# Optimization experiments

Hardware: AMD Instinct MI355X
Metric: run time of the kernel (lower is better)

## Reference

```python
import jax, jax.numpy as jnp
import numpy as np

B, T, F = 512, 1024, 8
H1, H2 = 70, 21   # '80k' config, bidirectional
D1, D2 = 30, 20


def _u(key, shape, fan):
    s = 1.0 / np.sqrt(fan)
    return jax.random.uniform(key, shape, jnp.float32, -s, s)


def setup_inputs() -> dict:
    key = jax.random.key(0)
    ks = iter(jax.random.split(key, 32))
    inp = {"x": jax.random.normal(next(ks), (B, T, F), jnp.float32)}
    # LSTM layer 1 (input F -> H1), forward and backward directions; torch gate order i,f,g,o
    for d in ("f", "b"):
        inp[f"w_ih1_{d}"] = _u(next(ks), (4 * H1, F), H1)
        inp[f"w_hh1_{d}"] = _u(next(ks), (4 * H1, H1), H1)
        inp[f"b_ih1_{d}"] = _u(next(ks), (4 * H1,), H1)
        inp[f"b_hh1_{d}"] = _u(next(ks), (4 * H1,), H1)
    # LSTM layer 2 (input 2*H1 -> H2)
    for d in ("f", "b"):
        inp[f"w_ih2_{d}"] = _u(next(ks), (4 * H2, 2 * H1), H2)
        inp[f"w_hh2_{d}"] = _u(next(ks), (4 * H2, H2), H2)
        inp[f"b_ih2_{d}"] = _u(next(ks), (4 * H2,), H2)
        inp[f"b_hh2_{d}"] = _u(next(ks), (4 * H2,), H2)
    # Dense head: 2*H2 -> D1 -> D2 -> 1
    inp["d1_w"] = _u(next(ks), (D1, 2 * H2), 2 * H2)
    inp["d1_b"] = _u(next(ks), (D1,), 2 * H2)
    inp["d2_w"] = _u(next(ks), (D2, D1), D1)
    inp["d2_b"] = _u(next(ks), (D2,), D1)
    inp["out_w"] = _u(next(ks), (1, D2), D2)
    inp["out_b"] = _u(next(ks), (1,), D2)
    return inp


def _lstm_dir(x, w_ih, w_hh, b_ih, b_hh, reverse):
    # x: [B, T, Fin]; torch LSTM gate order: i, f, g, o
    if reverse:
        x = x[:, ::-1]
    H = w_hh.shape[1]
    pre = jnp.einsum('btf,gf->btg', x, w_ih) + b_ih + b_hh  # [B, T, 4H]
    pre_t = jnp.moveaxis(pre, 1, 0)                          # [T, B, 4H]

    def step(carry, p):
        h, c = carry
        g = p + h @ w_hh.T
        i, f, gg, o = jnp.split(g, 4, axis=-1)
        c = jax.nn.sigmoid(f) * c + jax.nn.sigmoid(i) * jnp.tanh(gg)
        h = jax.nn.sigmoid(o) * jnp.tanh(c)
        return (h, c), h

    init = (jnp.zeros((x.shape[0], H), x.dtype), jnp.zeros((x.shape[0], H), x.dtype))
    _, hs = jax.lax.scan(step, init, pre_t)
    hs = jnp.moveaxis(hs, 0, 1)  # [B, T, H]
    if reverse:
        hs = hs[:, ::-1]
    return hs


def _bilstm(x, wf, uf, bif, bhf, wb, ub, bib, bhb):
    return jnp.concatenate([
        _lstm_dir(x, wf, uf, bif, bhf, reverse=False),
        _lstm_dir(x, wb, ub, bib, bhb, reverse=True),
    ], axis=-1)


def reference(x,
              w_ih1_f, w_hh1_f, b_ih1_f, b_hh1_f,
              w_ih1_b, w_hh1_b, b_ih1_b, b_hh1_b,
              w_ih2_f, w_hh2_f, b_ih2_f, b_hh2_f,
              w_ih2_b, w_hh2_b, b_ih2_b, b_hh2_b,
              d1_w, d1_b, d2_w, d2_b, out_w, out_b):
    h = _bilstm(x, w_ih1_f, w_hh1_f, b_ih1_f, b_hh1_f,
                w_ih1_b, w_hh1_b, b_ih1_b, b_hh1_b)   # [B, T, 2*H1]
    h = _bilstm(h, w_ih2_f, w_hh2_f, b_ih2_f, b_hh2_f,
                w_ih2_b, w_hh2_b, b_ih2_b, b_hh2_b)   # [B, T, 2*H2]
    h = jax.nn.relu(h @ d1_w.T + d1_b)
    h = jax.nn.relu(h @ d2_w.T + d2_b)
    return h @ out_w.T + out_b                          # [B, T, 1]
```

## Files before the change

kernel.cpp:

```cpp
#include <hip/hip_runtime.h>


typedef _Float16 v2f16 __attribute__((ext_vector_type(2)));
typedef _Float16 v4h   __attribute__((ext_vector_type(4)));
typedef _Float16 v8h   __attribute__((ext_vector_type(8)));
typedef float    f32x4 __attribute__((ext_vector_type(4)));

__device__ __forceinline__ float fdot2(v2f16 a, v2f16 b, float c) {
  return __builtin_amdgcn_fdot2(a, b, c, false);
}
#if __has_builtin(__builtin_amdgcn_rcpf)
__device__ __forceinline__ float rcpf(float x) { return __builtin_amdgcn_rcpf(x); }
#else
__device__ __forceinline__ float rcpf(float x) { return 1.f / x; }
#endif
__device__ __forceinline__ float ex2(float v) {
#if __has_builtin(__builtin_amdgcn_exp2f)
  return __builtin_amdgcn_exp2f(v);
#else
  return __expf(v * 0.6931471805599453f);
#endif
}

__device__ __forceinline__ void lds_barrier() {
  asm volatile("s_waitcnt lgkmcnt(0)" ::: "memory");
  __builtin_amdgcn_s_barrier();
  __builtin_amdgcn_sched_barrier(0);
}

#define O_W1M  0u
#define O_WP2  110592u
#define O_W2M  118656u
#define O_BIAS 177792u
#define O_DATA 178496u

__global__ void pack_kernel(const float* __restrict__ wihf, const float* __restrict__ whhf,
                            const float* __restrict__ wihb, const float* __restrict__ whhb,
                            const float* __restrict__ b1if, const float* __restrict__ b1hf,
                            const float* __restrict__ b1ib, const float* __restrict__ b1hb,
                            const float* __restrict__ wih2f, const float* __restrict__ wih2b,
                            const float* __restrict__ whh2f, const float* __restrict__ whh2b,
                            const float* __restrict__ bif, const float* __restrict__ bhf,
                            const float* __restrict__ bib, const float* __restrict__ bhb,
                            char* __restrict__ ws) {
  _Float16* w1m = (_Float16*)(ws + O_W1M);
  _Float16* wp2 = (_Float16*)(ws + O_WP2);
  _Float16* w2m = (_Float16*)(ws + O_W2M);
  float* biasc = (float*)(ws + O_BIAS);
  int idx = blockIdx.x * 256 + threadIdx.x;
  if (idx < 55296) {
    int d = idx / 27648, rem = idx % 27648, rp = rem / 96, k = rem % 96;
    int u = rp >> 2, g = rp & 3;
    const float* wih = d ? wihb : wihf;
    const float* whh = d ? whhb : whhf;
    const float* bi = d ? b1ib : b1if;
    const float* bh = d ? b1hb : b1hf;
    float v = 0.f;
    if (u < 70) {
      int src = g * 70 + u;
      float scale = (g == 2) ? 2.8853900817779268f : 1.4426950408889634f;
      if (k < 8) v = wih[src * 8 + k] * scale;
      else if (k < 78) v = whh[src * 70 + (k - 8)] * scale;
      else if (k == 78) v = (bi[src] + bh[src]) * scale;
    }
    w1m[idx] = (_Float16)v;
  } else if (idx < 59328) {
    int j = idx - 55296;
    int d = j / 2016, rem = j % 2016, r = rem / 24, k = rem % 24;
    const float* whh = d ? whh2b : whh2f;
    wp2[j] = (_Float16)((k < 21) ? whh[r * 21 + k] : 0.f);
  } else if (idx < 88896) {
    int j = idx - 59328;
    int n = j / 168, k = j % 168;
    float v = 0.f;
    if (k < 140) {
      if (n < 84) v = wih2f[n * 140 + k];
      else if (n < 168) v = wih2b[(n - 84) * 140 + k];
    }
    w2m[j] = (_Float16)v;
  } else if (idx < 89072) {
    int n = idx - 88896;
    float v = 0.f;
    if (n < 84) v = bif[n] + bhf[n];
    else if (n < 168) v = bib[n - 84] + bhb[n - 84];
    biasc[n] = v;
  }
}

__global__ __launch_bounds__(768) void lstm1_kernel(
    const float* __restrict__ x,
    const _Float16* __restrict__ w1m,
    _Float16* __restrict__ h1, int b0, int nb) {
  __shared__ __align__(16) _Float16 km[2][16][104];
  const int tid = threadIdx.x;
  const int w = tid >> 6, lane = tid & 63;
  const int q = lane >> 4, bc = lane & 15;
  const int d = blockIdx.y;
  const int blg = blockIdx.x * 16;
  const int gb0 = b0 + blg;

  for (int i = tid; i < 2 * 16 * 104; i += 768) ((_Float16*)km)[i] = (_Float16)0.f;

  int nt, T0;
  if (w < 4)       { nt = 1; T0 = w; }
  else if (w < 10) { nt = 2; T0 = 4 + 2 * (w - 4); }
  else             { nt = 1; T0 = 16 + (w - 10); }

  v8h af[2][3];
#pragma unroll
  for (int i = 0; i < 2; ++i) {
    if (i < nt) {
      int T = T0 + i;
#pragma unroll
      for (int kc = 0; kc < 3; ++kc)
        af[i][kc] = *(const v8h*)&w1m[(size_t)(d * 288 + T * 16 + bc) * 96 + kc * 32 + q * 8];
    }
  }

  __syncthreads();

  if (tid < 16) {
    km[0][tid][78] = (_Float16)1.f;
    km[1][tid][78] = (_Float16)1.f;
  }
  if (tid < 32) {
    int b = tid >> 1, half = tid & 1;
    int t0 = d ? 1023 : 0;
    float4 xv = *(const float4*)&x[((size_t)(gb0 + b) * 1024 + t0) * 8 + half * 4];
    v4h xh; xh[0] = (_Float16)xv.x; xh[1] = (_Float16)xv.y;
    xh[2] = (_Float16)xv.z; xh[3] = (_Float16)xv.w;
    *(v4h*)&km[0][b][half * 4] = xh;
  }
  float c0 = 0.f, c1 = 0.f;
  __syncthreads();

#pragma unroll 1
  for (int s = 0; s < 1024; ++s) {
    const int cur = s & 1, nxt = cur ^ 1;
    float4 xv;
    const bool xl = (tid < 32) && (s < 1023);
    if (xl) {
      int tn = d ? (1022 - s) : (s + 1);
      xv = *(const float4*)&x[((size_t)(gb0 + (tid >> 1)) * 1024 + tn) * 8 + (tid & 1) * 4];
    }
    v8h bf0 = *(const v8h*)&km[cur][bc][q * 8];
    v8h bf1 = *(const v8h*)&km[cur][bc][32 + q * 8];
    v8h bf2 = *(const v8h*)&km[cur][bc][64 + q * 8];
    f32x4 z4 = (f32x4){0.f, 0.f, 0.f, 0.f};
    f32x4 A0 = __builtin_amdgcn_mfma_f32_16x16x32_f16(af[0][0], bf0, z4, 0, 0, 0);
    f32x4 A1 = z4;
    if (nt == 2) A1 = __builtin_amdgcn_mfma_f32_16x16x32_f16(af[1][0], bf0, z4, 0, 0, 0);
    A0 = __builtin_amdgcn_mfma_f32_16x16x32_f16(af[0][1], bf1, A0, 0, 0, 0);
    if (nt == 2) A1 = __builtin_amdgcn_mfma_f32_16x16x32_f16(af[1][1], bf1, A1, 0, 0, 0);
    A0 = __builtin_amdgcn_mfma_f32_16x16x32_f16(af[0][2], bf2, A0, 0, 0, 0);
    if (nt == 2) A1 = __builtin_amdgcn_mfma_f32_16x16x32_f16(af[1][2], bf2, A1, 0, 0, 0);
    const int te = d ? (1023 - s) : s;
    const size_t rowb = ((size_t)te * nb + blg + bc) * 176 + d * 70;

#define GATE(Ai, ci, U)                                                      \
    {                                                                        \
      float ei = ex2(-Ai[0]);                                                \
      float ef = ex2(-Ai[1]);                                                \
      float eg = ex2(-Ai[2]);                                                \
      float eo = ex2(-Ai[3]);                                                \
      float si = rcpf(1.f + ei);                                             \
      float sf = rcpf(1.f + ef);                                             \
      float tg = fmaf(2.f, rcpf(1.f + eg), -1.f);                            \
      float so = rcpf(1.f + eo);                                             \
      ci = fmaf(sf, ci, si * tg);                                            \
      float ec = ex2(ci * -2.8853900817779268f);                             \
      float hv = so * fmaf(2.f, rcpf(1.f + ec), -1.f);                       \
      if ((U) < 70) {                                                        \
        _Float16 hh = (_Float16)hv;                                          \
        km[nxt][bc][8 + (U)] = hh;                                           \
        h1[rowb + (U)] = hh;                                                 \
      }                                                                      \
    }
    GATE(A0, c0, T0 * 4 + q)
    if (nt == 2) GATE(A1, c1, (T0 + 1) * 4 + q)
#undef GATE
    if (xl) {
      v4h xh; xh[0] = (_Float16)xv.x; xh[1] = (_Float16)xv.y;
      xh[2] = (_Float16)xv.z; xh[3] = (_Float16)xv.w;
      *(v4h*)&km[nxt][tid >> 1][(tid & 1) * 4] = xh;
    }
    lds_barrier();
  }
}

__global__ __launch_bounds__(256) void pre2_kernel(
    _Float16* __restrict__ h1, const char* __restrict__ ws) {
  const _Float16* w2m = (const _Float16*)(ws + O_W2M);
  const float* biasc = (const float*)(ws + O_BIAS);
  __shared__ _Float16 Al[64][184];
  __shared__ float Bl[176];
  const int tid = threadIdx.x;
  const int r0 = blockIdx.x * 64;
#pragma unroll
  for (int i = 0; i < 6; ++i) {
    int cid = i * 256 + tid;
    if (cid < 1408) {
      int row = cid / 22, ch = cid % 22;
      *(v8h*)&Al[row][ch * 8] = *(const v8h*)&h1[(size_t)(r0 + row) * 176 + ch * 8];
    }
  }
  if (tid < 176) Bl[tid] = biasc[tid];
  __syncthreads();

  const int wv = tid >> 6, lane = tid & 63;
  const int ml = lane & 15, kq = lane >> 4;
  v8h af[5];
#pragma unroll
  for (int k = 0; k < 4; ++k)
    af[k] = *(const v8h*)&Al[wv * 16 + ml][k * 32 + kq * 8];
  {
    v8h a4 = *(const v8h*)&Al[wv * 16 + ml][128 + kq * 8];
    if (kq >= 2) {
#pragma unroll
      for (int j = 0; j < 8; ++j) a4[j] = (_Float16)0.f;
    } else if (kq == 1) {
#pragma unroll
      for (int j = 4; j < 8; ++j) a4[j] = (_Float16)0.f;
    }
    af[4] = a4;
  }

  const v8h* wg = (const v8h*)w2m;
  f32x4 acc[11];
#pragma unroll
  for (int ct = 0; ct < 11; ++ct) acc[ct] = (f32x4){0.f, 0.f, 0.f, 0.f};

  v8h bc[5], bn[5];
#pragma unroll
  for (int k = 0; k < 5; ++k) bn[k] = wg[(size_t)ml * 21 + k * 4 + kq];
#pragma unroll
  for (int ct = 0; ct < 11; ++ct) {
#pragma unroll
    for (int k = 0; k < 5; ++k) bc[k] = bn[k];
    if (ct < 10) {
#pragma unroll
      for (int k = 0; k < 5; ++k) bn[k] = wg[(size_t)((ct + 1) * 16 + ml) * 21 + k * 4 + kq];
    }
#pragma unroll
    for (int k = 0; k < 5; ++k)
      acc[ct] = __builtin_amdgcn_mfma_f32_16x16x32_f16(af[k], bc[k], acc[ct], 0, 0, 0);
  }
  __syncthreads();
#pragma unroll
  for (int ct = 0; ct < 11; ++ct) {
#pragma unroll
    for (int r = 0; r < 4; ++r) {
      int row = wv * 16 + kq * 4 + r, col = ct * 16 + ml;
      Al[row][col] = (_Float16)(acc[ct][r] + Bl[col]);
    }
  }
  __syncthreads();
#pragma unroll
  for (int i = 0; i < 6; ++i) {
    int cid = i * 256 + tid;
    if (cid < 1408) {
      int row = cid / 22, ch = cid % 22;
      *(v8h*)&h1[(size_t)(r0 + row) * 176 + ch * 8] = *(const v8h*)&Al[row][ch * 8];
    }
  }
}

__global__ __launch_bounds__(64) void lstm2_kernel(
    const _Float16* __restrict__ pre2, const _Float16* __restrict__ wp2,
    _Float16* __restrict__ h2, int nb) {
  __shared__ __align__(16) _Float16 kv[2][32];
  const int lane = threadIdx.x;
  const int bl = blockIdx.x;
  const int d = blockIdx.y;
  const int u = lane >> 1, p = lane & 1;
  const bool active = lane < 42;

  ((_Float16*)kv)[lane] = (_Float16)0.f;

  v2f16 w0[12], w1[12];
  if (active) {
    const v8h* wr0 = (const v8h*)&wp2[(d * 84 + (2 * p) * 21 + u) * 24];
    const v8h* wr1 = (const v8h*)&wp2[(d * 84 + (2 * p + 1) * 21 + u) * 24];
#pragma unroll
    for (int ch = 0; ch < 3; ++ch) {
      v8h a = wr0[ch], b = wr1[ch];
#pragma unroll
      for (int q = 0; q < 4; ++q) {
        v2f16 t0; t0[0] = a[2 * q]; t0[1] = a[2 * q + 1]; w0[ch * 4 + q] = t0;
        v2f16 t1; t1[0] = b[2 * q]; t1[1] = b[2 * q + 1]; w1[ch * 4 + q] = t1;
      }
    }
  }
  const int col0 = d * 84 + (2 * p) * 21 + u;
  const int col1 = col0 + 21;
  const ptrdiff_t dlt = (ptrdiff_t)(d ? -nb : nb) * 176;
  const _Float16* pp = pre2 + ((size_t)(d ? 1023 : 0) * (size_t)nb + bl) * 176;

  _Float16 pa0 = pp[col0],            pa1 = pp[col1];
  _Float16 pb0 = (pp + dlt)[col0],    pb1 = (pp + dlt)[col1];
  _Float16 pc0 = (pp + 2*dlt)[col0],  pc1 = (pp + 2*dlt)[col1];
  _Float16 pd0 = (pp + 3*dlt)[col0],  pd1 = (pp + 3*dlt)[col1];
  const _Float16* pf = pp + 4 * dlt;

  const float esc0 = p ? -2.f : -1.f;
  const float ym0  = p ?  2.f :  1.f;
  const float ya0  = p ? -1.f :  0.f;
  float cc = 0.f;
  int s = 0;

#define L2STEP(P0, P1)                                                      \
  {                                                                         \
    const int cur = s & 1, nxt = cur ^ 1;                                   \
    float A0v = (float)P0, A1v = (float)P1;                                 \
    const float4* kp = (const float4*)&kv[cur][0];                          \
    float4 q0 = kp[0], q1 = kp[1], q2 = kp[2];                              \
    float x0 = A0v, x1 = 0.f, x2 = 0.f, x3 = 0.f;                           \
    float z0 = A1v, z1 = 0.f, z2 = 0.f, z3 = 0.f;                           \
    x0 = fdot2(__builtin_bit_cast(v2f16, q0.x), w0[0], x0);                 \
    x1 = fdot2(__builtin_bit_cast(v2f16, q0.y), w0[1], x1);                 \
    x2 = fdot2(__builtin_bit_cast(v2f16, q0.z), w0[2], x2);                 \
    x3 = fdot2(__builtin_bit_cast(v2f16, q0.w), w0[3], x3);                 \
    x0 = fdot2(__builtin_bit_cast(v2f16, q1.x), w0[4], x0);                 \
    x1 = fdot2(__builtin_bit_cast(v2f16, q1.y), w0[5], x1);                 \
    x2 = fdot2(__builtin_bit_cast(v2f16, q1.z), w0[6], x2);                 \
    x3 = fdot2(__builtin_bit_cast(v2f16, q1.w), w0[7], x3);                 \
    x0 = fdot2(__builtin_bit_cast(v2f16, q2.x), w0[8], x0);                 \
    x1 = fdot2(__builtin_bit_cast(v2f16, q2.y), w0[9], x1);                 \
    x2 = fdot2(__builtin_bit_cast(v2f16, q2.z), w0[10], x2);                \
    x3 = fdot2(__builtin_bit_cast(v2f16, q2.w), w0[11], x3);                \
    z0 = fdot2(__builtin_bit_cast(v2f16, q0.x), w1[0], z0);                 \
    z1 = fdot2(__builtin_bit_cast(v2f16, q0.y), w1[1], z1);                 \
    z2 = fdot2(__builtin_bit_cast(v2f16, q0.z), w1[2], z2);                 \
    z3 = fdot2(__builtin_bit_cast(v2f16, q0.w), w1[3], z3);                 \
    z0 = fdot2(__builtin_bit_cast(v2f16, q1.x), w1[4], z0);                 \
    z1 = fdot2(__builtin_bit_cast(v2f16, q1.y), w1[5], z1);                 \
    z2 = fdot2(__builtin_bit_cast(v2f16, q1.z), w1[6], z2);                 \
    z3 = fdot2(__builtin_bit_cast(v2f16, q1.w), w1[7], z3);                 \
    z0 = fdot2(__builtin_bit_cast(v2f16, q2.x), w1[8], z0);                 \
    z1 = fdot2(__builtin_bit_cast(v2f16, q2.y), w1[9], z1);                 \
    z2 = fdot2(__builtin_bit_cast(v2f16, q2.z), w1[10], z2);                \
    z3 = fdot2(__builtin_bit_cast(v2f16, q2.w), w1[11], z3);                \
    float A = (x0 + x1) + (x2 + x3), Bv = (z0 + z1) + (z2 + z3);            \
    float Y0 = fmaf(ym0, rcpf(1.f + __expf(A * esc0)), ya0);                \
    float Y1 = rcpf(1.f + __expf(-Bv));                                     \
    float Zs = __shfl_xor(Y0, 1);                                           \
    float Ws = __shfl_xor(Y1, 1);                                           \
    float ai = p ? Zs : Y0;                                                 \
    float af = p ? Ws : Y1;                                                 \
    float ag = p ? Y0 : Zs;                                                 \
    float ao = p ? Y1 : Ws;                                                 \
    cc = fmaf(af, cc, ai * ag);                                             \
    float tc = fmaf(2.f, rcpf(1.f + __expf(-2.f * cc)), -1.f);              \
    float hv = ao * tc;                                                     \
    if (active && p == 0) {                                                 \
      _Float16 hh = (_Float16)hv;                                           \
      int te = d ? (1023 - s) : s;                                          \
      kv[nxt][u] = hh;                                                      \
      h2[((size_t)te * nb + bl) * 48 + d * 21 + u] = hh;                    \
    }                                                                       \
    if (s < 1020) { P0 = pf[col0]; P1 = pf[col1]; }                         \
    pf += dlt;                                                              \
    ++s;                                                                    \
  }

#pragma unroll 1
  for (int it = 0; it < 256; ++it) {
    L2STEP(pa0, pa1)
    L2STEP(pb0, pb1)
    L2STEP(pc0, pc1)
    L2STEP(pd0, pd1)
  }
#undef L2STEP
}

__global__ __launch_bounds__(256) void head_kernel(
    const _Float16* __restrict__ h2,
    const float* __restrict__ d1w, const float* __restrict__ d1b,
    const float* __restrict__ d2w, const float* __restrict__ d2b,
    const float* __restrict__ ow, const float* __restrict__ ob,
    float* __restrict__ out, int b0, int lognb) {
  int n = blockIdx.x * 256 + threadIdx.x;
  int t = n >> lognb, bl = n & ((1 << lognb) - 1);
  const v8h* hp = (const v8h*)&h2[(size_t)n * 48];
  float in[48];
#pragma unroll
  for (int i = 0; i < 6; ++i) {
    v8h hc = hp[i];
#pragma unroll
    for (int j = 0; j < 8; ++j) in[i * 8 + j] = (float)hc[j];
  }
  float a1[30];
#pragma unroll
  for (int cc = 0; cc < 30; ++cc) {
    float a = d1b[cc];
#pragma unroll
    for (int k = 0; k < 42; ++k) a += in[k] * d1w[cc * 42 + k];
    a1[cc] = fmaxf(a, 0.f);
  }
  float a2[20];
#pragma unroll
  for (int cc = 0; cc < 20; ++cc) {
    float a = d2b[cc];
#pragma unroll
    for (int k = 0; k < 30; ++k) a += a1[k] * d2w[cc * 30 + k];
    a2[cc] = fmaxf(a, 0.f);
  }
  float o = ob[0];
#pragma unroll
  for (int k = 0; k < 20; ++k) o += a2[k] * ow[k];
  out[(size_t)(b0 + bl) * 1024 + t] = o;
}

extern "C" void kernel_launch(void* const* d_in, const int* in_sizes, int n_in,
                              void* d_out, int out_size, void* d_ws, size_t ws_size,
                              hipStream_t stream) {
  const float* x = (const float*)d_in[0];
  const float* wih1f = (const float*)d_in[1];
  const float* whh1f = (const float*)d_in[2];
  const float* bih1f = (const float*)d_in[3];
  const float* bhh1f = (const float*)d_in[4];
  const float* wih1b = (const float*)d_in[5];
  const float* whh1b = (const float*)d_in[6];
  const float* bih1b = (const float*)d_in[7];
  const float* bhh1b = (const float*)d_in[8];
  const float* wih2f = (const float*)d_in[9];
  const float* whh2f = (const float*)d_in[10];
  const float* bih2f = (const float*)d_in[11];
  const float* bhh2f = (const float*)d_in[12];
  const float* wih2b = (const float*)d_in[13];
  const float* whh2b = (const float*)d_in[14];
  const float* bih2b = (const float*)d_in[15];
  const float* bhh2b = (const float*)d_in[16];
  const float* d1w = (const float*)d_in[17];
  const float* d1b = (const float*)d_in[18];
  const float* d2w = (const float*)d_in[19];
  const float* d2b = (const float*)d_in[20];
  const float* ow = (const float*)d_in[21];
  const float* ob = (const float*)d_in[22];
  float* out = (float*)d_out;
  char* wsb = (char*)d_ws;

  const int cands[6] = {1, 2, 4, 8, 16, 32};
  int nslice = 32;
  for (int i = 0; i < 6; ++i) {
    size_t rows = (size_t)(512 / cands[i]) * 1024;
    if (O_DATA + rows * 448 <= ws_size) { nslice = cands[i]; break; }
  }
  const int nb = 512 / nslice;
  int lognb = 0; while ((1 << lognb) < nb) ++lognb;
  const size_t rows = (size_t)nb * 1024;

  _Float16* w1m = (_Float16*)(wsb + O_W1M);
  _Float16* wp2 = (_Float16*)(wsb + O_WP2);
  _Float16* h1  = (_Float16*)(wsb + O_DATA);
  _Float16* h2  = (_Float16*)(wsb + O_DATA + rows * 352);

  pack_kernel<<<348, 256, 0, stream>>>(wih1f, whh1f, wih1b, whh1b,
                                       bih1f, bhh1f, bih1b, bhh1b,
                                       wih2f, wih2b, whh2f, whh2b,
                                       bih2f, bhh2f, bih2b, bhh2b, wsb);

  for (int s = 0; s < nslice; ++s) {
    const int b0 = s * nb;
    lstm1_kernel<<<dim3(nb / 16, 2), 768, 0, stream>>>(x, w1m, h1, b0, nb);
    pre2_kernel<<<nb * 16, 256, 0, stream>>>(h1, wsb);
    lstm2_kernel<<<dim3(nb, 2), 64, 0, stream>>>(h1, wp2, h2, nb);
    head_kernel<<<nb * 4, 256, 0, stream>>>(h2, d1w, d1b, d2w, d2b, ow, ob,
                                            out, b0, lognb);
  }
}
```

Before: 1.383 ms.

## Widen LSTM1 to 16 waves, pre-scale layer-2 gates by log2e, use DPP shuffles

Layer 1 now runs 1024 threads (16 waves), with only two waves computing two gate tiles instead of six, which shortens the per-step critical path. The x-prefetch lanes move to a late wave. Layer 2 weights and biases are pre-scaled by log2e (2·log2e for the g gate) and interleaved per unit, so the activations use exp2 directly and each pre-activation pair loads as a single half2. The cross-lane __shfl_xor is replaced with a DPP quad permute. The larger block raises register pressure, and the layout change depends on pre2 producing the new interleaved column order.

```diff
diff --git a/kernel.cpp b/kernel.cpp
--- a/kernel.cpp
+++ b/kernel.cpp
@@ -21,12 +21,20 @@
   return __expf(v * 0.6931471805599453f);
 #endif
 }
+__device__ __forceinline__ float dpp_xor1(float v) {
+  return __builtin_bit_cast(float,
+      __builtin_amdgcn_update_dpp(0, __builtin_bit_cast(int, v),
+                                  0xB1 , 0xF, 0xF, true));
+}
 
 __device__ __forceinline__ void lds_barrier() {
   asm volatile("s_waitcnt lgkmcnt(0)" ::: "memory");
   __builtin_amdgcn_s_barrier();
   __builtin_amdgcn_sched_barrier(0);
 }
+
+#define LOG2E  1.4426950408889634f
+#define LOG2E2 2.8853900817779268f
 
 #define O_W1M  0u
 #define O_WP2  110592u
@@ -58,7 +66,7 @@
     float v = 0.f;
     if (u < 70) {
       int src = g * 70 + u;
-      float scale = (g == 2) ? 2.8853900817779268f : 1.4426950408889634f;
+      float scale = (g == 2) ? LOG2E2 : LOG2E;
       if (k < 8) v = wih[src * 8 + k] * scale;
       else if (k < 78) v = whh[src * 70 + (k - 8)] * scale;
       else if (k == 78) v = (bi[src] + bh[src]) * scale;
@@ -68,26 +76,34 @@
     int j = idx - 55296;
     int d = j / 2016, rem = j % 2016, r = rem / 24, k = rem % 24;
     const float* whh = d ? whh2b : whh2f;
-    wp2[j] = (_Float16)((k < 21) ? whh[r * 21 + k] : 0.f);
+    float scale = (r / 21 == 2) ? LOG2E2 : LOG2E;
+    wp2[j] = (_Float16)((k < 21) ? whh[r * 21 + k] * scale : 0.f);
   } else if (idx < 88896) {
     int j = idx - 59328;
     int n = j / 168, k = j % 168;
     float v = 0.f;
-    if (k < 140) {
-      if (n < 84) v = wih2f[n * 140 + k];
-      else if (n < 168) v = wih2b[(n - 84) * 140 + k];
+    if (n < 168 && k < 140) {
+      int d = n / 84, m = n % 84, u = m >> 2, g = m & 3;
+      const float* wih = d ? wih2b : wih2f;
+      float scale = (g == 2) ? LOG2E2 : LOG2E;
+      v = wih[(g * 21 + u) * 140 + k] * scale;
     }
     w2m[j] = (_Float16)v;
   } else if (idx < 89072) {
     int n = idx - 88896;
     float v = 0.f;
-    if (n < 84) v = bif[n] + bhf[n];
-    else if (n < 168) v = bib[n - 84] + bhb[n - 84];
+    if (n < 168) {
+      int d = n / 84, m = n % 84, u = m >> 2, g = m & 3;
+      const float* bi = d ? bib : bif;
+      const float* bh = d ? bhb : bhf;
+      float scale = (g == 2) ? LOG2E2 : LOG2E;
+      v = (bi[g * 21 + u] + bh[g * 21 + u]) * scale;
+    }
     biasc[n] = v;
   }
 }
 
-__global__ __launch_bounds__(768) void lstm1_kernel(
+__global__ __launch_bounds__(1024) void lstm1_kernel(
     const float* __restrict__ x,
     const _Float16* __restrict__ w1m,
     _Float16* __restrict__ h1, int b0, int nb) {
@@ -99,22 +115,19 @@
   const int blg = blockIdx.x * 16;
   const int gb0 = b0 + blg;
 
-  for (int i = tid; i < 2 * 16 * 104; i += 768) ((_Float16*)km)[i] = (_Float16)0.f;
-
-  int nt, T0;
-  if (w < 4)       { nt = 1; T0 = w; }
-  else if (w < 10) { nt = 2; T0 = 4 + 2 * (w - 4); }
-  else             { nt = 1; T0 = 16 + (w - 10); }
+  for (int i = tid; i < 2 * 16 * 104; i += 1024) ((_Float16*)km)[i] = (_Float16)0.f;
+
+  const bool two = (w < 2);
+  const int T0 = two ? 2 * w : 2 + w;
 
   v8h af[2][3];
 #pragma unroll
-  for (int i = 0; i < 2; ++i) {
-    if (i < nt) {
-      int T = T0 + i;
-#pragma unroll
-      for (int kc = 0; kc < 3; ++kc)
-        af[i][kc] = *(const v8h*)&w1m[(size_t)(d * 288 + T * 16 + bc) * 96 + kc * 32 + q * 8];
-    }
+  for (int kc = 0; kc < 3; ++kc)
+    af[0][kc] = *(const v8h*)&w1m[(size_t)(d * 288 + T0 * 16 + bc) * 96 + kc * 32 + q * 8];
+  if (two) {
+#pragma unroll
+    for (int kc = 0; kc < 3; ++kc)
+      af[1][kc] = *(const v8h*)&w1m[(size_t)(d * 288 + (T0 + 1) * 16 + bc) * 96 + kc * 32 + q * 8];
   }
 
   __syncthreads();
@@ -123,8 +136,9 @@
     km[0][tid][78] = (_Float16)1.f;
     km[1][tid][78] = (_Float16)1.f;
   }
-  if (tid < 32) {
-    int b = tid >> 1, half = tid & 1;
+  const bool xlane = (tid >= 960 && tid < 992);
+  if (xlane) {
+    int b = (tid - 960) >> 1, half = (tid - 960) & 1;
     int t0 = d ? 1023 : 0;
     float4 xv = *(const float4*)&x[((size_t)(gb0 + b) * 1024 + t0) * 8 + half * 4];
     v4h xh; xh[0] = (_Float16)xv.x; xh[1] = (_Float16)xv.y;
@@ -138,10 +152,10 @@
   for (int s = 0; s < 1024; ++s) {
     const int cur = s & 1, nxt = cur ^ 1;
     float4 xv;
-    const bool xl = (tid < 32) && (s < 1023);
+    const bool xl = xlane && (s < 1023);
     if (xl) {
       int tn = d ? (1022 - s) : (s + 1);
-      xv = *(const float4*)&x[((size_t)(gb0 + (tid >> 1)) * 1024 + tn) * 8 + (tid & 1) * 4];
+      xv = *(const float4*)&x[((size_t)(gb0 + ((tid - 960) >> 1)) * 1024 + tn) * 8 + ((tid - 960) & 1) * 4];
     }
     v8h bf0 = *(const v8h*)&km[cur][bc][q * 8];
     v8h bf1 = *(const v8h*)&km[cur][bc][32 + q * 8];
@@ -149,11 +163,11 @@
     f32x4 z4 = (f32x4){0.f, 0.f, 0.f, 0.f};
     f32x4 A0 = __builtin_amdgcn_mfma_f32_16x16x32_f16(af[0][0], bf0, z4, 0, 0, 0);
     f32x4 A1 = z4;
-    if (nt == 2) A1 = __builtin_amdgcn_mfma_f32_16x16x32_f16(af[1][0], bf0, z4, 0, 0, 0);
+    if (two) A1 = __builtin_amdgcn_mfma_f32_16x16x32_f16(af[1][0], bf0, z4, 0, 0, 0);
     A0 = __builtin_amdgcn_mfma_f32_16x16x32_f16(af[0][1], bf1, A0, 0, 0, 0);
-    if (nt == 2) A1 = __builtin_amdgcn_mfma_f32_16x16x32_f16(af[1][1], bf1, A1, 0, 0, 0);
+    if (two) A1 = __builtin_amdgcn_mfma_f32_16x16x32_f16(af[1][1], bf1, A1, 0, 0, 0);
     A0 = __builtin_amdgcn_mfma_f32_16x16x32_f16(af[0][2], bf2, A0, 0, 0, 0);
-    if (nt == 2) A1 = __builtin_amdgcn_mfma_f32_16x16x32_f16(af[1][2], bf2, A1, 0, 0, 0);
+    if (two) A1 = __builtin_amdgcn_mfma_f32_16x16x32_f16(af[1][2], bf2, A1, 0, 0, 0);
     const int te = d ? (1023 - s) : s;
     const size_t rowb = ((size_t)te * nb + blg + bc) * 176 + d * 70;
 
@@ -168,7 +182,7 @@
       float tg = fmaf(2.f, rcpf(1.f + eg), -1.f);                            \
       float so = rcpf(1.f + eo);                                             \
       ci = fmaf(sf, ci, si * tg);                                            \
-      float ec = ex2(ci * -2.8853900817779268f);                             \
+      float ec = ex2(ci * -LOG2E2);                                          \
       float hv = so * fmaf(2.f, rcpf(1.f + ec), -1.f);                       \
       if ((U) < 70) {                                                        \
         _Float16 hh = (_Float16)hv;                                          \
@@ -177,12 +191,12 @@
       }                                                                      \
     }
     GATE(A0, c0, T0 * 4 + q)
-    if (nt == 2) GATE(A1, c1, (T0 + 1) * 4 + q)
+    if (two) GATE(A1, c1, (T0 + 1) * 4 + q)
 #undef GATE
     if (xl) {
       v4h xh; xh[0] = (_Float16)xv.x; xh[1] = (_Float16)xv.y;
       xh[2] = (_Float16)xv.z; xh[3] = (_Float16)xv.w;
-      *(v4h*)&km[nxt][tid >> 1][(tid & 1) * 4] = xh;
+      *(v4h*)&km[nxt][(tid - 960) >> 1][((tid - 960) & 1) * 4] = xh;
     }
     lds_barrier();
   }
@@ -291,27 +305,23 @@
       }
     }
   }
-  const int col0 = d * 84 + (2 * p) * 21 + u;
-  const int col1 = col0 + 21;
+  const int cp = d * 84 + u * 4 + 2 * p;
   const ptrdiff_t dlt = (ptrdiff_t)(d ? -nb : nb) * 176;
   const _Float16* pp = pre2 + ((size_t)(d ? 1023 : 0) * (size_t)nb + bl) * 176;
 
-  _Float16 pa0 = pp[col0],            pa1 = pp[col1];
-  _Float16 pb0 = (pp + dlt)[col0],    pb1 = (pp + dlt)[col1];
-  _Float16 pc0 = (pp + 2*dlt)[col0],  pc1 = (pp + 2*dlt)[col1];
-  _Float16 pd0 = (pp + 3*dlt)[col0],  pd1 = (pp + 3*dlt)[col1];
+  v2f16 pa = *(const v2f16*)(pp + cp);
+  v2f16 pb = *(const v2f16*)(pp + dlt + cp);
+  v2f16 pc = *(const v2f16*)(pp + 2 * dlt + cp);
+  v2f16 pd = *(const v2f16*)(pp + 3 * dlt + cp);
   const _Float16* pf = pp + 4 * dlt;
 
-  const float esc0 = p ? -2.f : -1.f;
-  const float ym0  = p ?  2.f :  1.f;
-  const float ya0  = p ? -1.f :  0.f;
   float cc = 0.f;
   int s = 0;
 
-#define L2STEP(P0, P1)                                                      \
+#define L2STEP(P)                                                           \
   {                                                                         \
     const int cur = s & 1, nxt = cur ^ 1;                                   \
-    float A0v = (float)P0, A1v = (float)P1;                                 \
+    float A0v = (float)P[0], A1v = (float)P[1];                             \
     const float4* kp = (const float4*)&kv[cur][0];                          \
     float4 q0 = kp[0], q1 = kp[1], q2 = kp[2];                              \
     float x0 = A0v, x1 = 0.f, x2 = 0.f, x3 = 0.f;                           \
@@ -341,16 +351,18 @@
     z2 = fdot2(__builtin_bit_cast(v2f16, q2.z), w1[10], z2);                \
     z3 = fdot2(__builtin_bit_cast(v2f16, q2.w), w1[11], z3);                \
     float A = (x0 + x1) + (x2 + x3), Bv = (z0 + z1) + (z2 + z3);            \
-    float Y0 = fmaf(ym0, rcpf(1.f + __expf(A * esc0)), ya0);                \
-    float Y1 = rcpf(1.f + __expf(-Bv));                                     \
-    float Zs = __shfl_xor(Y0, 1);                                           \
-    float Ws = __shfl_xor(Y1, 1);                                           \
+            \
+    float r0v = rcpf(1.f + ex2(-A));                                        \
+    float Y0 = p ? fmaf(2.f, r0v, -1.f) : r0v;                              \
+    float Y1 = rcpf(1.f + ex2(-Bv));                                        \
+    float Zs = dpp_xor1(Y0);                                                \
+    float Ws = dpp_xor1(Y1);                                                \
     float ai = p ? Zs : Y0;                                                 \
     float af = p ? Ws : Y1;                                                 \
     float ag = p ? Y0 : Zs;                                                 \
     float ao = p ? Y1 : Ws;                                                 \
     cc = fmaf(af, cc, ai * ag);                                             \
-    float tc = fmaf(2.f, rcpf(1.f + __expf(-2.f * cc)), -1.f);              \
+    float tc = fmaf(2.f, rcpf(1.f + ex2(cc * -LOG2E2)), -1.f);              \
     float hv = ao * tc;                                                     \
     if (active && p == 0) {                                                 \
       _Float16 hh = (_Float16)hv;                                           \
@@ -358,17 +370,17 @@
       kv[nxt][u] = hh;                                                      \
       h2[((size_t)te * nb + bl) * 48 + d * 21 + u] = hh;                    \
     }                                                                       \
-    if (s < 1020) { P0 = pf[col0]; P1 = pf[col1]; }                         \
+    if (s < 1020) P = *(const v2f16*)(pf + cp);                             \
     pf += dlt;                                                              \
     ++s;                                                                    \
   }
 
 #pragma unroll 1
   for (int it = 0; it < 256; ++it) {
-    L2STEP(pa0, pa1)
-    L2STEP(pb0, pb1)
-    L2STEP(pc0, pc1)
-    L2STEP(pd0, pd1)
+    L2STEP(pa)
+    L2STEP(pb)
+    L2STEP(pc)
+    L2STEP(pd)
   }
 #undef L2STEP
 }
@@ -462,7 +474,7 @@
 
   for (int s = 0; s < nslice; ++s) {
     const int b0 = s * nb;
-    lstm1_kernel<<<dim3(nb / 16, 2), 768, 0, stream>>>(x, w1m, h1, b0, nb);
+    lstm1_kernel<<<dim3(nb / 16, 2), 1024, 0, stream>>>(x, w1m, h1, b0, nb);
     pre2_kernel<<<nb * 16, 256, 0, stream>>>(h1, wsb);
     lstm2_kernel<<<dim3(nb, 2), 64, 0, stream>>>(h1, wp2, h2, nb);
     head_kernel<<<nb * 4, 256, 0, stream>>>(h2, d1w, d1b, d2w, d2b, ow, ob,
```

Result: faster. 1.329 ms (-3.9%).
